# Optimization experiments

Measured on AMD Instinct MI355X. Metric: run time of the kernel, lower is better.

## Reference

```python
import jax, jax.numpy as jnp
import numpy as np

B, S = 64, 1024
ATTEND_DIM = QUERY_DIM = ATT_DIM = 1024


def setup_inputs() -> dict:
    key = jax.random.key(0)
    ks = jax.random.split(key, 8)
    sc_pre = 1.0 / np.sqrt(ATTEND_DIM)
    sc_q = 1.0 / np.sqrt(QUERY_DIM)
    sc_v = 1.0 / np.sqrt(ATT_DIM)
    return {
        "input": jax.random.normal(ks[0], (B, QUERY_DIM), jnp.float32),
        "context": jax.random.normal(ks[1], (B, S, ATTEND_DIM), jnp.float32),
        "coverage_acc": jax.random.uniform(ks[2], (B, S), jnp.float32),
        "W_pre": jax.random.normal(ks[3], (ATT_DIM, ATTEND_DIM), jnp.float32) * sc_pre,
        "b_pre": jax.random.normal(ks[4], (ATT_DIM,), jnp.float32) * sc_pre,
        "W_q": jax.random.normal(ks[5], (ATT_DIM, QUERY_DIM), jnp.float32) * sc_q,
        "W_v": jax.random.normal(ks[6], (1, ATT_DIM), jnp.float32) * sc_v,
        "W_cov": jax.random.normal(ks[7], (ATT_DIM, 1), jnp.float32),
    }


def reference(input, context, coverage_acc, W_pre, b_pre, W_q, W_v, W_cov):
    # precompute = linear_pre(context): (B, S, att_dim)
    precompute = jnp.einsum('bsa,da->bsd', context, W_pre) + b_pre
    # targetT = linear_q(input): (B, 1, att_dim)
    targetT = (input @ W_q.T)[:, None, :]
    # coverage contribution: linear_cov(coverage[..., None]) -> (B, S, att_dim)
    cov_term = coverage_acc[..., None] * W_cov[:, 0]
    tmp = jnp.tanh(precompute + targetT + cov_term)
    # energy = linear_v(tanh(...)): (B, S)
    energy = jnp.einsum('bsd,d->bs', tmp, W_v[0])
    score = jax.nn.softmax(energy, axis=1)
    coverage_new = coverage_acc + score
    weightedContext = jnp.einsum('bs,bsa->ba', score, context)
    return (weightedContext, score, coverage_new, precompute)
```

## Files before the change

kernel.cpp:

```cpp
#include <hip/hip_runtime.h>
#include <hip/hip_bf16.h>

#define B_  64
#define S_  1024
#define D_  1024
#define K_  1024

typedef unsigned short u16;
typedef short bf16x8 __attribute__((ext_vector_type(8)));
typedef float f32x4  __attribute__((ext_vector_type(4)));
typedef u16   u16x8  __attribute__((ext_vector_type(8)));
typedef u16   u16x4  __attribute__((ext_vector_type(4)));

#define WS_TARGET 0
#define WS_EPART  262144
#define WS_WCPART 2359296
#define WS_WPRE   6553600
#define WS_CTXBF  8650752
#define WS_NEED_BF 142868480ull

__device__ __forceinline__ u16 f2bf(float f) {
    unsigned u = __float_as_uint(f);
    return (u16)((u + 0x7fffu + ((u >> 16) & 1u)) >> 16);
}
__device__ __forceinline__ float bf2f(u16 h) {
    return __uint_as_float(((unsigned)h) << 16);
}
__device__ __forceinline__ float fast_tanh(float x) {
    float t = __expf(2.0f * x);
    return 1.0f - 2.0f * __builtin_amdgcn_rcpf(t + 1.0f);
}

__device__ __forceinline__ void glds16(const void* g, void* l) {
    __builtin_amdgcn_global_load_lds(
        (__attribute__((address_space(1))) void*)(size_t)g,
        (__attribute__((address_space(3))) void*)(unsigned int)(size_t)l,
        16, 0, 0);
}

__global__ void convert_bf16x8_kernel(const float* __restrict__ src, u16* __restrict__ dst) {
    size_t i = ((size_t)blockIdx.x * 256 + threadIdx.x) * 8;
    float4 a = *reinterpret_cast<const float4*>(src + i);
    float4 b = *reinterpret_cast<const float4*>(src + i + 4);
    u16x8 h = { f2bf(a.x), f2bf(a.y), f2bf(a.z), f2bf(a.w),
                f2bf(b.x), f2bf(b.y), f2bf(b.z), f2bf(b.w) };
    *reinterpret_cast<u16x8*>(dst + i) = h;
}

__global__ void target_kernel(const float* __restrict__ inp, const float* __restrict__ wq,
                              float* __restrict__ target) {
    int tid  = threadIdx.x;
    int lane = tid & 63, wid = tid >> 6;
    int pair = blockIdx.x * 4 + wid;
    int b = pair & 63, n = pair >> 6;
    const float* ir = inp + (size_t)b * K_;
    const float* wr = wq  + (size_t)n * K_;
    float acc = 0.f;
#pragma unroll
    for (int jj = 0; jj < 4; ++jj) {
        int off = jj * 256 + lane * 4;
        float4 a = *reinterpret_cast<const float4*>(ir + off);
        float4 w = *reinterpret_cast<const float4*>(wr + off);
        acc += a.x * w.x + a.y * w.y + a.z * w.z + a.w * w.w;
    }
#pragma unroll
    for (int off = 1; off < 64; off <<= 1) acc += __shfl_xor(acc, off);
    if (lane == 0) target[pair] = acc;
}

__global__ __launch_bounds__(256, 2)
void gemm_ep_fast(const u16* __restrict__ ctxb, const u16* __restrict__ wpre,
                  const float* __restrict__ bpre, const float* __restrict__ wv,
                  const float* __restrict__ wcov, const float* __restrict__ target,
                  const float* __restrict__ cov, float* __restrict__ pre_out,
                  float* __restrict__ epart) {
    __shared__ __align__(16) u16 As[256 * 32];
    __shared__ __align__(16) u16 Bs[128 * 32];
    __shared__ float esm[256];

    const int tid  = threadIdx.x;
    const int lane = tid & 63;
    const int wid  = tid >> 6;
    const int wm = wid >> 1, wn = wid & 1;
    const int lr = lane & 15, quad = lane >> 4;
    const int m_base = blockIdx.y * 256;
    const int n_base = blockIdx.x * 128;
    const int b      = m_base >> 10;
    const int s_base = m_base & 1023;

    const int srow = lane >> 2;
    const int scol = (lane & 3) * 8;
    const u16* gA = ctxb + (size_t)(m_base + wid * 64 + srow) * K_ + scol;
    const u16* gB = wpre + (size_t)(n_base + wid * 32 + srow) * K_ + scol;
    u16* lA = &As[(wid * 64) * 32];
    u16* lB = &Bs[(wid * 32) * 32];

    f32x4 acc[8][4];
#pragma unroll
    for (int i = 0; i < 8; ++i)
#pragma unroll
        for (int j = 0; j < 4; ++j) acc[i][j] = (f32x4){0.f, 0.f, 0.f, 0.f};

    esm[tid] = 0.0f;

    for (int kt = 0; kt < 32; ++kt) {
        const int k0 = kt * 32;
#pragma unroll
        for (int c = 0; c < 4; ++c)
            glds16(gA + (size_t)(c * 16) * K_ + k0, lA + c * 16 * 32);
#pragma unroll
        for (int c = 0; c < 2; ++c)
            glds16(gB + (size_t)(c * 16) * K_ + k0, lB + c * 16 * 32);
        __syncthreads();

        bf16x8 af[8], bfr[4];
#pragma unroll
        for (int i = 0; i < 8; ++i)
            af[i] = *reinterpret_cast<const bf16x8*>(&As[(wm * 128 + i * 16 + lr) * 32 + quad * 8]);
#pragma unroll
        for (int j = 0; j < 4; ++j)
            bfr[j] = *reinterpret_cast<const bf16x8*>(&Bs[(wn * 64 + j * 16 + lr) * 32 + quad * 8]);
#pragma unroll
        for (int i = 0; i < 8; ++i)
#pragma unroll
            for (int j = 0; j < 4; ++j)
                acc[i][j] = __builtin_amdgcn_mfma_f32_16x16x32_bf16(af[i], bfr[j], acc[i][j], 0, 0, 0);
        __syncthreads();
    }

    float bpre_j[4], wv_j[4], wcov_j[4], tgt_j[4];
    int n_j[4];
#pragma unroll
    for (int j = 0; j < 4; ++j) {
        n_j[j]    = n_base + wn * 64 + j * 16 + lr;
        bpre_j[j] = bpre[n_j[j]];
        wv_j[j]   = wv[n_j[j]];
        wcov_j[j] = wcov[n_j[j]];
        tgt_j[j]  = target[n_j[j] * 64 + b];
    }
#pragma unroll
    for (int i = 0; i < 8; ++i) {
#pragma unroll
        for (int r = 0; r < 4; ++r) {
            int row_local = wm * 128 + i * 16 + quad * 4 + r;
            int m = m_base + row_local;
            int s = s_base + row_local;
            float c = cov[b * S_ + s];
            float esum = 0.f;
#pragma unroll
            for (int j = 0; j < 4; ++j) {
                float pre = acc[i][j][r] + bpre_j[j];
                __builtin_nontemporal_store(pre, &pre_out[(size_t)m * D_ + n_j[j]]);
                float t = fast_tanh(pre + tgt_j[j] + c * wcov_j[j]);
                esum += t * wv_j[j];
            }
            esum += __shfl_xor(esum, 1);
            esum += __shfl_xor(esum, 2);
            esum += __shfl_xor(esum, 4);
            esum += __shfl_xor(esum, 8);
            if (lr == 0) atomicAdd(&esm[row_local], esum);
        }
    }
    __syncthreads();
    epart[(size_t)(m_base + tid) * 8 + blockIdx.x] = esm[tid];
}

#define LDA 40
__global__ __launch_bounds__(256, 2)
void gemm_ep_fallback(const float* __restrict__ ctxf, const u16* __restrict__ wpre,
                      const float* __restrict__ bpre, const float* __restrict__ wv,
                      const float* __restrict__ wcov, const float* __restrict__ target,
                      const float* __restrict__ cov, float* __restrict__ pre_out,
                      float* __restrict__ epart) {
    __shared__ __align__(16) u16 As[256 * LDA];
    __shared__ __align__(16) u16 Bs[128 * LDA];
    __shared__ float esm[256];
    const int tid  = threadIdx.x;
    const int lane = tid & 63;
    const int wid  = tid >> 6;
    const int wm = wid >> 1, wn = wid & 1;
    const int lr = lane & 15, quad = lane >> 4;
    const int m_base = blockIdx.y * 256;
    const int n_base = blockIdx.x * 128;
    const int b      = m_base >> 10;
    const int s_base = m_base & 1023;

    f32x4 acc[8][4];
#pragma unroll
    for (int i = 0; i < 8; ++i)
#pragma unroll
        for (int j = 0; j < 4; ++j) acc[i][j] = (f32x4){0.f, 0.f, 0.f, 0.f};
    esm[tid] = 0.0f;

    for (int kt = 0; kt < 32; ++kt) {
        const int k0 = kt * 32;
        {
            const int row0 = tid >> 3, kc = (tid & 7) * 4;
#pragma unroll
            for (int p = 0; p < 8; ++p) {
                int row = row0 + p * 32;
                float4 v = *reinterpret_cast<const float4*>(
                    ctxf + (size_t)(m_base + row) * K_ + k0 + kc);
                u16x4 h = { f2bf(v.x), f2bf(v.y), f2bf(v.z), f2bf(v.w) };
                *reinterpret_cast<u16x4*>(&As[row * LDA + kc]) = h;
            }
        }
        {
            const int row0 = tid >> 2, kc = (tid & 3) * 8;
#pragma unroll
            for (int p = 0; p < 2; ++p) {
                int row = row0 + p * 64;
                u16x8 v = *reinterpret_cast<const u16x8*>(
                    wpre + (size_t)(n_base + row) * K_ + k0 + kc);
                *reinterpret_cast<u16x8*>(&Bs[row * LDA + kc]) = v;
            }
        }
        __syncthreads();
        bf16x8 af[8], bfr[4];
#pragma unroll
        for (int i = 0; i < 8; ++i)
            af[i] = *reinterpret_cast<const bf16x8*>(&As[(wm * 128 + i * 16 + lr) * LDA + quad * 8]);
#pragma unroll
        for (int j = 0; j < 4; ++j)
            bfr[j] = *reinterpret_cast<const bf16x8*>(&Bs[(wn * 64 + j * 16 + lr) * LDA + quad * 8]);
#pragma unroll
        for (int i = 0; i < 8; ++i)
#pragma unroll
            for (int j = 0; j < 4; ++j)
                acc[i][j] = __builtin_amdgcn_mfma_f32_16x16x32_bf16(af[i], bfr[j], acc[i][j], 0, 0, 0);
        __syncthreads();
    }
    float bpre_j[4], wv_j[4], wcov_j[4], tgt_j[4];
    int n_j[4];
#pragma unroll
    for (int j = 0; j < 4; ++j) {
        n_j[j]    = n_base + wn * 64 + j * 16 + lr;
        bpre_j[j] = bpre[n_j[j]];
        wv_j[j]   = wv[n_j[j]];
        wcov_j[j] = wcov[n_j[j]];
        tgt_j[j]  = target[n_j[j] * 64 + b];
    }
#pragma unroll
    for (int i = 0; i < 8; ++i) {
#pragma unroll
        for (int r = 0; r < 4; ++r) {
            int row_local = wm * 128 + i * 16 + quad * 4 + r;
            int m = m_base + row_local;
            int s = s_base + row_local;
            float c = cov[b * S_ + s];
            float esum = 0.f;
#pragma unroll
            for (int j = 0; j < 4; ++j) {
                float pre = acc[i][j][r] + bpre_j[j];
                __builtin_nontemporal_store(pre, &pre_out[(size_t)m * D_ + n_j[j]]);
                float t = fast_tanh(pre + tgt_j[j] + c * wcov_j[j]);
                esum += t * wv_j[j];
            }
            esum += __shfl_xor(esum, 1);
            esum += __shfl_xor(esum, 2);
            esum += __shfl_xor(esum, 4);
            esum += __shfl_xor(esum, 8);
            if (lr == 0) atomicAdd(&esm[row_local], esum);
        }
    }
    __syncthreads();
    epart[(size_t)(m_base + tid) * 8 + blockIdx.x] = esm[tid];
}

__global__ void softmax_cov_kernel(const float* __restrict__ epart, const float* __restrict__ cov,
                                   float* __restrict__ score, float* __restrict__ covnew) {
    int b = blockIdx.x, t = threadIdx.x;
    int lane = t & 63, wid = t >> 6;
    __shared__ float red[4];
    float e[4];
    float lmax = -3.4e38f;
#pragma unroll
    for (int p = 0; p < 4; ++p) {
        int s = p * 256 + t;
        const float4* q = reinterpret_cast<const float4*>(epart + (size_t)(b * S_ + s) * 8);
        float4 a = q[0], c = q[1];
        e[p] = a.x + a.y + a.z + a.w + c.x + c.y + c.z + c.w;
        lmax = fmaxf(lmax, e[p]);
    }
#pragma unroll
    for (int off = 1; off < 64; off <<= 1) lmax = fmaxf(lmax, __shfl_xor(lmax, off));
    if (lane == 0) red[wid] = lmax;
    __syncthreads();
    float bm = fmaxf(fmaxf(red[0], red[1]), fmaxf(red[2], red[3]));
    __syncthreads();
    float ex[4];
    float lsum = 0.f;
#pragma unroll
    for (int p = 0; p < 4; ++p) { ex[p] = __expf(e[p] - bm); lsum += ex[p]; }
#pragma unroll
    for (int off = 1; off < 64; off <<= 1) lsum += __shfl_xor(lsum, off);
    if (lane == 0) red[wid] = lsum;
    __syncthreads();
    float total = red[0] + red[1] + red[2] + red[3];
    float inv = __builtin_amdgcn_rcpf(total);
#pragma unroll
    for (int p = 0; p < 4; ++p) {
        int s = p * 256 + t;
        float sc = ex[p] * inv;
        score[b * S_ + s]  = sc;
        covnew[b * S_ + s] = cov[b * S_ + s] + sc;
    }
}

__global__ void wc_partial_bf(const float* __restrict__ score, const u16* __restrict__ ctxb,
                              float* __restrict__ part) {
    int sp = blockIdx.x, b = blockIdx.y, t = threadIdx.x;
    int col = t * 4;
    float ax = 0.f, ay = 0.f, az = 0.f, aw = 0.f;
    const u16*   base  = ctxb + ((size_t)b * S_ + sp * 64) * K_ + col;
    const float* sbase = score + b * S_ + sp * 64;
    for (int ss = 0; ss < 64; ++ss) {
        float w = sbase[ss];
        u16x4 c = *reinterpret_cast<const u16x4*>(base + (size_t)ss * K_);
        ax += w * bf2f(c[0]); ay += w * bf2f(c[1]);
        az += w * bf2f(c[2]); aw += w * bf2f(c[3]);
    }
    float4 o = { ax, ay, az, aw };
    *reinterpret_cast<float4*>(part + (size_t)(b * 16 + sp) * 1024 + col) = o;
}

__global__ void wc_partial_f32(const float* __restrict__ score, const float* __restrict__ ctx,
                               float* __restrict__ part) {
    int sp = blockIdx.x, b = blockIdx.y, t = threadIdx.x;
    int col = t * 4;
    float ax = 0.f, ay = 0.f, az = 0.f, aw = 0.f;
    const float* base  = ctx + ((size_t)b * S_ + sp * 64) * K_ + col;
    const float* sbase = score + b * S_ + sp * 64;
    for (int ss = 0; ss < 64; ++ss) {
        float w = sbase[ss];
        float4 c = *reinterpret_cast<const float4*>(base + (size_t)ss * K_);
        ax += w * c.x; ay += w * c.y; az += w * c.z; aw += w * c.w;
    }
    float4 o = { ax, ay, az, aw };
    *reinterpret_cast<float4*>(part + (size_t)(b * 16 + sp) * 1024 + col) = o;
}

__global__ void wc_reduce_kernel(const float* __restrict__ part, float* __restrict__ wc) {
    int b = blockIdx.x, t = threadIdx.x;
    int col = t * 4;
    float ax = 0.f, ay = 0.f, az = 0.f, aw = 0.f;
#pragma unroll
    for (int p = 0; p < 16; ++p) {
        float4 v = *reinterpret_cast<const float4*>(part + (size_t)(b * 16 + p) * 1024 + col);
        ax += v.x; ay += v.y; az += v.z; aw += v.w;
    }
    float4 o = { ax, ay, az, aw };
    *reinterpret_cast<float4*>(wc + b * 1024 + col) = o;
}

extern "C" void kernel_launch(void* const* d_in, const int* in_sizes, int n_in,
                              void* d_out, int out_size, void* d_ws, size_t ws_size,
                              hipStream_t stream) {
    const float* input = (const float*)d_in[0];
    const float* ctx   = (const float*)d_in[1];
    const float* cov   = (const float*)d_in[2];
    const float* Wpre  = (const float*)d_in[3];
    const float* bpre  = (const float*)d_in[4];
    const float* Wq    = (const float*)d_in[5];
    const float* Wv    = (const float*)d_in[6];
    const float* Wcov  = (const float*)d_in[7];

    float* out        = (float*)d_out;
    float* out_wc     = out;
    float* out_score  = out + 65536;
    float* out_covnew = out + 131072;
    float* out_pre    = out + 196608;

    char*  ws        = (char*)d_ws;
    float* ws_target = (float*)(ws + WS_TARGET);
    float* ws_epart  = (float*)(ws + WS_EPART);
    float* ws_wcpart = (float*)(ws + WS_WCPART);
    u16*   ws_wpre   = (u16*)(ws + WS_WPRE);
    u16*   ws_ctxbf  = (u16*)(ws + WS_CTXBF);

    const bool use_bf = (ws_size >= WS_NEED_BF);

    convert_bf16x8_kernel<<<512, 256, 0, stream>>>(Wpre, ws_wpre);
    if (use_bf)
        convert_bf16x8_kernel<<<32768, 256, 0, stream>>>(ctx, ws_ctxbf);
    target_kernel<<<16384, 256, 0, stream>>>(input, Wq, ws_target);
    dim3 ggrid(8, 256);
    if (use_bf)
        gemm_ep_fast<<<ggrid, 256, 0, stream>>>(ws_ctxbf, ws_wpre, bpre, Wv, Wcov,
                                                ws_target, cov, out_pre, ws_epart);
    else
        gemm_ep_fallback<<<ggrid, 256, 0, stream>>>(ctx, ws_wpre, bpre, Wv, Wcov,
                                                    ws_target, cov, out_pre, ws_epart);
    softmax_cov_kernel<<<64, 256, 0, stream>>>(ws_epart, cov, out_score, out_covnew);
    if (use_bf)
        wc_partial_bf<<<dim3(16, 64), 256, 0, stream>>>(out_score, ws_ctxbf, ws_wcpart);
    else
        wc_partial_f32<<<dim3(16, 64), 256, 0, stream>>>(out_score, ctx, ws_wcpart);
    wc_reduce_kernel<<<64, 256, 0, stream>>>(ws_wcpart, out_wc);
}
```

Measured before the change: 694.2 us.

## Double-buffer LDS tiles in fast GEMM and remap blocks for XCD locality

Splits the shared-memory A/B tiles into two buffers so the global-to-LDS load of the next K tile is issued before the MFMA work on the current one. This hides load latency and halves the barriers per K step. It also switches to a 1D grid whose block index is remapped so that the eight N-tiles of one M-tile share an XCD, improving L2 reuse of the context rows. LDS use doubles, which may reduce occupancy under the 2-blocks-per-SM launch bound.

```diff
diff --git a/kernel.cpp b/kernel.cpp
--- a/kernel.cpp
+++ b/kernel.cpp
@@ -74,8 +74,10 @@
                   const float* __restrict__ wcov, const float* __restrict__ target,
                   const float* __restrict__ cov, float* __restrict__ pre_out,
                   float* __restrict__ epart) {
-    __shared__ __align__(16) u16 As[256 * 32];
-    __shared__ __align__(16) u16 Bs[128 * 32];
+    __shared__ __align__(16) u16 As0[256 * 32];
+    __shared__ __align__(16) u16 As1[256 * 32];
+    __shared__ __align__(16) u16 Bs0[128 * 32];
+    __shared__ __align__(16) u16 Bs1[128 * 32];
     __shared__ float esm[256];
 
     const int tid  = threadIdx.x;
@@ -83,8 +85,14 @@
     const int wid  = tid >> 6;
     const int wm = wid >> 1, wn = wid & 1;
     const int lr = lane & 15, quad = lane >> 4;
-    const int m_base = blockIdx.y * 256;
-    const int n_base = blockIdx.x * 128;
+
+    const int lin  = blockIdx.x;
+    const int xcd  = lin & 7;
+    const int slot = lin >> 3;
+    const int mt   = (slot >> 3) * 8 + xcd;
+    const int nt   = slot & 7;
+    const int m_base = mt * 256;
+    const int n_base = nt * 128;
     const int b      = m_base >> 10;
     const int s_base = m_base & 1023;
 
@@ -92,8 +100,10 @@
     const int scol = (lane & 3) * 8;
     const u16* gA = ctxb + (size_t)(m_base + wid * 64 + srow) * K_ + scol;
     const u16* gB = wpre + (size_t)(n_base + wid * 32 + srow) * K_ + scol;
-    u16* lA = &As[(wid * 64) * 32];
-    u16* lB = &Bs[(wid * 32) * 32];
+    u16* lA0 = &As0[(wid * 64) * 32];
+    u16* lA1 = &As1[(wid * 64) * 32];
+    u16* lB0 = &Bs0[(wid * 32) * 32];
+    u16* lB1 = &Bs1[(wid * 32) * 32];
 
     f32x4 acc[8][4];
 #pragma unroll
@@ -103,30 +113,40 @@
 
     esm[tid] = 0.0f;
 
-    for (int kt = 0; kt < 32; ++kt) {
-        const int k0 = kt * 32;
-#pragma unroll
-        for (int c = 0; c < 4; ++c)
-            glds16(gA + (size_t)(c * 16) * K_ + k0, lA + c * 16 * 32);
-#pragma unroll
-        for (int c = 0; c < 2; ++c)
-            glds16(gB + (size_t)(c * 16) * K_ + k0, lB + c * 16 * 32);
+#define STAGE_(k0, lA_, lB_) do {                                              \
+    _Pragma("unroll") for (int c = 0; c < 4; ++c)                              \
+        glds16(gA + (size_t)(c * 16) * K_ + (k0), (lA_) + c * 16 * 32);        \
+    _Pragma("unroll") for (int c = 0; c < 2; ++c)                              \
+        glds16(gB + (size_t)(c * 16) * K_ + (k0), (lB_) + c * 16 * 32);        \
+} while (0)
+
+#define COMPUTE_(AsB, BsB) do {                                                \
+    bf16x8 af[8], bfr[4];                                                      \
+    _Pragma("unroll") for (int i = 0; i < 8; ++i)                              \
+        af[i] = *reinterpret_cast<const bf16x8*>(                              \
+            &(AsB)[(wm * 128 + i * 16 + lr) * 32 + quad * 8]);                 \
+    _Pragma("unroll") for (int j = 0; j < 4; ++j)                              \
+        bfr[j] = *reinterpret_cast<const bf16x8*>(                             \
+            &(BsB)[(wn * 64 + j * 16 + lr) * 32 + quad * 8]);                  \
+    _Pragma("unroll") for (int i = 0; i < 8; ++i)                              \
+        _Pragma("unroll") for (int j = 0; j < 4; ++j)                          \
+            acc[i][j] = __builtin_amdgcn_mfma_f32_16x16x32_bf16(               \
+                af[i], bfr[j], acc[i][j], 0, 0, 0);                            \
+} while (0)
+
+    STAGE_(0, lA0, lB0);
+    __syncthreads();
+
+    for (int kt = 0; kt < 32; kt += 2) {
+        STAGE_((kt + 1) * 32, lA1, lB1);
+        COMPUTE_(As0, Bs0);
         __syncthreads();
-
-        bf16x8 af[8], bfr[4];
-#pragma unroll
-        for (int i = 0; i < 8; ++i)
-            af[i] = *reinterpret_cast<const bf16x8*>(&As[(wm * 128 + i * 16 + lr) * 32 + quad * 8]);
-#pragma unroll
-        for (int j = 0; j < 4; ++j)
-            bfr[j] = *reinterpret_cast<const bf16x8*>(&Bs[(wn * 64 + j * 16 + lr) * 32 + quad * 8]);
-#pragma unroll
-        for (int i = 0; i < 8; ++i)
-#pragma unroll
-            for (int j = 0; j < 4; ++j)
-                acc[i][j] = __builtin_amdgcn_mfma_f32_16x16x32_bf16(af[i], bfr[j], acc[i][j], 0, 0, 0);
+        if (kt < 30) STAGE_((kt + 2) * 32, lA0, lB0);
+        COMPUTE_(As1, Bs1);
         __syncthreads();
     }
+#undef STAGE_
+#undef COMPUTE_
 
     float bpre_j[4], wv_j[4], wcov_j[4], tgt_j[4];
     int n_j[4];
@@ -162,7 +182,7 @@
         }
     }
     __syncthreads();
-    epart[(size_t)(m_base + tid) * 8 + blockIdx.x] = esm[tid];
+    epart[(size_t)(m_base + tid) * 8 + nt] = esm[tid];
 }
 
 #define LDA 40
@@ -384,13 +404,14 @@
     if (use_bf)
         convert_bf16x8_kernel<<<32768, 256, 0, stream>>>(ctx, ws_ctxbf);
     target_kernel<<<16384, 256, 0, stream>>>(input, Wq, ws_target);
-    dim3 ggrid(8, 256);
     if (use_bf)
-        gemm_ep_fast<<<ggrid, 256, 0, stream>>>(ws_ctxbf, ws_wpre, bpre, Wv, Wcov,
-                                                ws_target, cov, out_pre, ws_epart);
-    else
+        gemm_ep_fast<<<2048, 256, 0, stream>>>(ws_ctxbf, ws_wpre, bpre, Wv, Wcov,
+                                               ws_target, cov, out_pre, ws_epart);
+    else {
+        dim3 ggrid(8, 256);
         gemm_ep_fallback<<<ggrid, 256, 0, stream>>>(ctx, ws_wpre, bpre, Wv, Wcov,
                                                     ws_target, cov, out_pre, ws_epart);
+    }
     softmax_cov_kernel<<<64, 256, 0, stream>>>(ws_epart, cov, out_score, out_covnew);
     if (use_bf)
         wc_partial_bf<<<dim3(16, 64), 256, 0, stream>>>(out_score, ws_ctxbf, ws_wcpart);
```

After: 659.6 us. -5.0%, faster.

## Shrink GEMM tile to 128x128, swizzle LDS, remap blocks across XCDs

Applied to the files above, without the earlier changes.

The fused GEMM+energy kernel drops from 256x128 to 128x128 output tiles and raises the occupancy hint to three blocks per SM. It adds an XOR swizzle on the LDS column index to cut bank conflicts on MFMA fragment loads. It also uses a 1D grid with an XCD-aware mapping so blocks sharing A rows run on the same XCD and reuse L2. Smaller tiles mean more loads of the B operand per FLOP but lower register pressure and better latency hiding.

```diff
diff --git a/kernel.cpp b/kernel.cpp
--- a/kernel.cpp
+++ b/kernel.cpp
@@ -68,63 +68,71 @@
     if (lane == 0) target[pair] = acc;
 }
 
-__global__ __launch_bounds__(256, 2)
+__global__ __launch_bounds__(256, 3)
 void gemm_ep_fast(const u16* __restrict__ ctxb, const u16* __restrict__ wpre,
                   const float* __restrict__ bpre, const float* __restrict__ wv,
                   const float* __restrict__ wcov, const float* __restrict__ target,
                   const float* __restrict__ cov, float* __restrict__ pre_out,
                   float* __restrict__ epart) {
-    __shared__ __align__(16) u16 As[256 * 32];
+    __shared__ __align__(16) u16 As[128 * 32];
     __shared__ __align__(16) u16 Bs[128 * 32];
-    __shared__ float esm[256];
+    __shared__ float esm[128];
 
     const int tid  = threadIdx.x;
     const int lane = tid & 63;
     const int wid  = tid >> 6;
     const int wm = wid >> 1, wn = wid & 1;
     const int lr = lane & 15, quad = lane >> 4;
-    const int m_base = blockIdx.y * 256;
-    const int n_base = blockIdx.x * 128;
+    const int sq = quad ^ ((lr >> 1) & 3);
+
+    const int lin  = blockIdx.x;
+    const int xcd  = lin & 7;
+    const int slot = lin >> 3;
+    const int mt   = (slot >> 3) * 8 + xcd;
+    const int nt   = slot & 7;
+    const int m_base = mt * 128;
+    const int n_base = nt * 128;
     const int b      = m_base >> 10;
     const int s_base = m_base & 1023;
 
     const int srow = lane >> 2;
-    const int scol = (lane & 3) * 8;
-    const u16* gA = ctxb + (size_t)(m_base + wid * 64 + srow) * K_ + scol;
+    const int scol = ((lane & 3) ^ ((lane >> 3) & 3)) * 8;
+    const u16* gA = ctxb + (size_t)(m_base + wid * 32 + srow) * K_ + scol;
     const u16* gB = wpre + (size_t)(n_base + wid * 32 + srow) * K_ + scol;
-    u16* lA = &As[(wid * 64) * 32];
+    u16* lA = &As[(wid * 32) * 32];
     u16* lB = &Bs[(wid * 32) * 32];
 
-    f32x4 acc[8][4];
-#pragma unroll
-    for (int i = 0; i < 8; ++i)
+    f32x4 acc[4][4];
+#pragma unroll
+    for (int i = 0; i < 4; ++i)
 #pragma unroll
         for (int j = 0; j < 4; ++j) acc[i][j] = (f32x4){0.f, 0.f, 0.f, 0.f};
 
-    esm[tid] = 0.0f;
+    if (tid < 128) esm[tid] = 0.0f;
 
     for (int kt = 0; kt < 32; ++kt) {
         const int k0 = kt * 32;
-#pragma unroll
-        for (int c = 0; c < 4; ++c)
-            glds16(gA + (size_t)(c * 16) * K_ + k0, lA + c * 16 * 32);
-#pragma unroll
-        for (int c = 0; c < 2; ++c)
-            glds16(gB + (size_t)(c * 16) * K_ + k0, lB + c * 16 * 32);
+        glds16(gA + k0,                      lA);
+        glds16(gA + (size_t)16 * K_ + k0,    lA + 16 * 32);
+        glds16(gB + k0,                      lB);
+        glds16(gB + (size_t)16 * K_ + k0,    lB + 16 * 32);
         __syncthreads();
 
-        bf16x8 af[8], bfr[4];
-#pragma unroll
-        for (int i = 0; i < 8; ++i)
-            af[i] = *reinterpret_cast<const bf16x8*>(&As[(wm * 128 + i * 16 + lr) * 32 + quad * 8]);
+        bf16x8 af[4], bfr[4];
+#pragma unroll
+        for (int i = 0; i < 4; ++i)
+            af[i] = *reinterpret_cast<const bf16x8*>(
+                &As[(wm * 64 + i * 16 + lr) * 32 + sq * 8]);
 #pragma unroll
         for (int j = 0; j < 4; ++j)
-            bfr[j] = *reinterpret_cast<const bf16x8*>(&Bs[(wn * 64 + j * 16 + lr) * 32 + quad * 8]);
-#pragma unroll
-        for (int i = 0; i < 8; ++i)
+            bfr[j] = *reinterpret_cast<const bf16x8*>(
+                &Bs[(wn * 64 + j * 16 + lr) * 32 + sq * 8]);
+#pragma unroll
+        for (int i = 0; i < 4; ++i)
 #pragma unroll
             for (int j = 0; j < 4; ++j)
-                acc[i][j] = __builtin_amdgcn_mfma_f32_16x16x32_bf16(af[i], bfr[j], acc[i][j], 0, 0, 0);
+                acc[i][j] = __builtin_amdgcn_mfma_f32_16x16x32_bf16(
+                    af[i], bfr[j], acc[i][j], 0, 0, 0);
         __syncthreads();
     }
 
@@ -139,10 +147,10 @@
         tgt_j[j]  = target[n_j[j] * 64 + b];
     }
 #pragma unroll
-    for (int i = 0; i < 8; ++i) {
+    for (int i = 0; i < 4; ++i) {
 #pragma unroll
         for (int r = 0; r < 4; ++r) {
-            int row_local = wm * 128 + i * 16 + quad * 4 + r;
+            int row_local = wm * 64 + i * 16 + quad * 4 + r;
             int m = m_base + row_local;
             int s = s_base + row_local;
             float c = cov[b * S_ + s];
@@ -162,7 +170,7 @@
         }
     }
     __syncthreads();
-    epart[(size_t)(m_base + tid) * 8 + blockIdx.x] = esm[tid];
+    if (tid < 128) epart[(size_t)(m_base + tid) * 8 + nt] = esm[tid];
 }
 
 #define LDA 40
@@ -384,13 +392,14 @@
     if (use_bf)
         convert_bf16x8_kernel<<<32768, 256, 0, stream>>>(ctx, ws_ctxbf);
     target_kernel<<<16384, 256, 0, stream>>>(input, Wq, ws_target);
-    dim3 ggrid(8, 256);
     if (use_bf)
-        gemm_ep_fast<<<ggrid, 256, 0, stream>>>(ws_ctxbf, ws_wpre, bpre, Wv, Wcov,
-                                                ws_target, cov, out_pre, ws_epart);
-    else
+        gemm_ep_fast<<<4096, 256, 0, stream>>>(ws_ctxbf, ws_wpre, bpre, Wv, Wcov,
+                                               ws_target, cov, out_pre, ws_epart);
+    else {
+        dim3 ggrid(8, 256);
         gemm_ep_fallback<<<ggrid, 256, 0, stream>>>(ctx, ws_wpre, bpre, Wv, Wcov,
                                                     ws_target, cov, out_pre, ws_epart);
+    }
     softmax_cov_kernel<<<64, 256, 0, stream>>>(ws_epart, cov, out_score, out_covnew);
     if (use_bf)
         wc_partial_bf<<<dim3(16, 64), 256, 0, stream>>>(out_score, ws_ctxbf, ws_wcpart);
```

New measurement: 669.4 us. 3.6% less time.

## Restructure fused GEMM into 256x256 double-buffered ping-pong pipeline with XCD-aware tiling

Applied to the files above, without the earlier changes.

The fused precompute GEMM+energy kernel moves to 512-thread blocks computing 256x256 tiles with K-step 64. The tiles are double-buffered in LDS with XOR-swizzled layout, and global-to-LDS loads are interleaved with MFMA phases using explicit barriers, waitcnt and setprio. Block IDs are remapped so consecutive M tiles are spread across XCDs for better L2 reuse of the B operand. This aims to hide load latency and cut LDS bank conflicts and global traffic. In exchange it brings heavy LDS use (128KB), fragile manual synchronization, and epart padding with zeros for unused slots.

```diff
diff --git a/kernel.cpp b/kernel.cpp
--- a/kernel.cpp
+++ b/kernel.cpp
@@ -68,32 +68,38 @@
     if (lane == 0) target[pair] = acc;
 }
 
-__global__ __launch_bounds__(256, 2)
+__global__ __launch_bounds__(512, 2)
 void gemm_ep_fast(const u16* __restrict__ ctxb, const u16* __restrict__ wpre,
                   const float* __restrict__ bpre, const float* __restrict__ wv,
                   const float* __restrict__ wcov, const float* __restrict__ target,
                   const float* __restrict__ cov, float* __restrict__ pre_out,
                   float* __restrict__ epart) {
-    __shared__ __align__(16) u16 As[256 * 32];
-    __shared__ __align__(16) u16 Bs[128 * 32];
+    __shared__ __align__(16) u16 A0[256 * 64];
+    __shared__ __align__(16) u16 A1[256 * 64];
+    __shared__ __align__(16) u16 B0[256 * 64];
+    __shared__ __align__(16) u16 B1[256 * 64];
     __shared__ float esm[256];
 
     const int tid  = threadIdx.x;
     const int lane = tid & 63;
     const int wid  = tid >> 6;
-    const int wm = wid >> 1, wn = wid & 1;
+    const int wm = wid >> 2, wn = wid & 3;
     const int lr = lane & 15, quad = lane >> 4;
-    const int m_base = blockIdx.y * 256;
-    const int n_base = blockIdx.x * 128;
+
+    const int lin  = blockIdx.x;
+    const int xcd  = lin & 7;
+    const int slot = lin >> 3;
+    const int nt   = slot & 3;
+    const int mt   = (slot >> 2) * 8 + xcd;
+    const int m_base = mt * 256;
+    const int n_base = nt * 256;
     const int b      = m_base >> 10;
     const int s_base = m_base & 1023;
 
-    const int srow = lane >> 2;
-    const int scol = (lane & 3) * 8;
-    const u16* gA = ctxb + (size_t)(m_base + wid * 64 + srow) * K_ + scol;
-    const u16* gB = wpre + (size_t)(n_base + wid * 32 + srow) * K_ + scol;
-    u16* lA = &As[(wid * 64) * 32];
-    u16* lB = &Bs[(wid * 32) * 32];
+    const int srow8 = lane >> 3;
+    const int scol  = ((lane & 7) ^ (lane >> 3)) * 8;
+    const u16* gA = ctxb + (size_t)(m_base + wid * 16 + srow8) * K_ + scol;
+    const u16* gB = wpre + (size_t)(n_base + wid * 16 + srow8) * K_ + scol;
 
     f32x4 acc[8][4];
 #pragma unroll
@@ -101,32 +107,94 @@
 #pragma unroll
         for (int j = 0; j < 4; ++j) acc[i][j] = (f32x4){0.f, 0.f, 0.f, 0.f};
 
-    esm[tid] = 0.0f;
-
-    for (int kt = 0; kt < 32; ++kt) {
-        const int k0 = kt * 32;
-#pragma unroll
-        for (int c = 0; c < 4; ++c)
-            glds16(gA + (size_t)(c * 16) * K_ + k0, lA + c * 16 * 32);
-#pragma unroll
-        for (int c = 0; c < 2; ++c)
-            glds16(gB + (size_t)(c * 16) * K_ + k0, lB + c * 16 * 32);
-        __syncthreads();
-
-        bf16x8 af[8], bfr[4];
-#pragma unroll
-        for (int i = 0; i < 8; ++i)
-            af[i] = *reinterpret_cast<const bf16x8*>(&As[(wm * 128 + i * 16 + lr) * 32 + quad * 8]);
-#pragma unroll
-        for (int j = 0; j < 4; ++j)
-            bfr[j] = *reinterpret_cast<const bf16x8*>(&Bs[(wn * 64 + j * 16 + lr) * 32 + quad * 8]);
-#pragma unroll
-        for (int i = 0; i < 8; ++i)
-#pragma unroll
-            for (int j = 0; j < 4; ++j)
-                acc[i][j] = __builtin_amdgcn_mfma_f32_16x16x32_bf16(af[i], bfr[j], acc[i][j], 0, 0, 0);
-        __syncthreads();
-    }
+#define STG(garr, R, kt_, larr) do {                                           \
+    glds16(garr + (size_t)(R) * K_ + (kt_) * 64,                               \
+           &larr[((R) + wid * 16 + 0) * 64]);                                  \
+    glds16(garr + (size_t)((R) + 8) * K_ + (kt_) * 64,                         \
+           &larr[((R) + wid * 16 + 8) * 64]);                                  \
+} while (0)
+
+#define LDA4(dst, arr, ibase, h)                                               \
+    _Pragma("unroll") for (int ii = 0; ii < 4; ++ii)                           \
+        dst[ii] = *reinterpret_cast<const bf16x8*>(                            \
+            &arr[(wm * 128 + ((ibase) + ii) * 16 + lr) * 64 +                  \
+                 ((((h) * 4 + quad) ^ (lr & 7)) * 8)]);
+#define LDB4(dst, arr, h)                                                      \
+    _Pragma("unroll") for (int jj = 0; jj < 4; ++jj)                           \
+        dst[jj] = *reinterpret_cast<const bf16x8*>(                            \
+            &arr[(wn * 64 + jj * 16 + lr) * 64 +                               \
+                 ((((h) * 4 + quad) ^ (lr & 7)) * 8)]);
+#define MFMA16(ibase, A4, B4)                                                  \
+    _Pragma("unroll") for (int ii = 0; ii < 4; ++ii)                           \
+        _Pragma("unroll") for (int jj = 0; jj < 4; ++jj)                       \
+            acc[(ibase) + ii][jj] = __builtin_amdgcn_mfma_f32_16x16x32_bf16(   \
+                A4[ii], B4[jj], acc[(ibase) + ii][jj], 0, 0, 0);
+
+#define PH_MID() do {                                                          \
+    __builtin_amdgcn_s_barrier();                                              \
+    asm volatile("s_waitcnt lgkmcnt(0)" ::: "memory");                         \
+    __builtin_amdgcn_sched_barrier(0);                                         \
+    __builtin_amdgcn_s_setprio(1);                                             \
+} while (0)
+#define PH_END() do {                                                          \
+    __builtin_amdgcn_s_setprio(0);                                             \
+    __builtin_amdgcn_s_barrier();                                              \
+    __builtin_amdgcn_sched_barrier(0);                                         \
+} while (0)
+#define PH_END_VM() do {                                                       \
+    __builtin_amdgcn_s_setprio(0);                                             \
+    asm volatile("s_waitcnt vmcnt(2)" ::: "memory");                           \
+    __builtin_amdgcn_s_barrier();                                              \
+    __builtin_amdgcn_sched_barrier(0);                                         \
+} while (0)
+
+    bf16x8 alo[4], ahi[4], bfv[4];
+
+    STG(gA, 0, 0, A0); STG(gA, 128, 0, A0);
+    STG(gB, 0, 0, B0); STG(gB, 128, 0, B0);
+    STG(gB, 0, 1, B1);
+    if (tid < 256) esm[tid] = 0.0f;
+    asm volatile("s_waitcnt vmcnt(2)" ::: "memory");
+    __builtin_amdgcn_s_barrier();
+    __builtin_amdgcn_sched_barrier(0);
+
+    for (int i = 0; i < 8; ++i) {
+        const int t1 = 2 * i + 1;
+        const int t2 = (2 * i + 2 < 16) ? 2 * i + 2 : 15;
+        const int t3 = (2 * i + 3 < 16) ? 2 * i + 3 : 15;
+        LDA4(alo, A0, 0, 0); LDB4(bfv, B0, 0);
+        STG(gA, 0, t1, A1);
+        PH_MID(); MFMA16(0, alo, bfv); PH_END();
+        LDA4(ahi, A0, 4, 0);
+        STG(gA, 128, t1, A1);
+        PH_MID(); MFMA16(4, ahi, bfv); PH_END();
+        LDA4(alo, A0, 0, 1); LDB4(bfv, B0, 1);
+        STG(gB, 128, t1, B1);
+        PH_MID(); MFMA16(0, alo, bfv); PH_END();
+        LDA4(ahi, A0, 4, 1);
+        STG(gB, 0, t2, B0);
+        PH_MID(); MFMA16(4, ahi, bfv); PH_END_VM();
+        LDA4(alo, A1, 0, 0); LDB4(bfv, B1, 0);
+        STG(gA, 0, t2, A0);
+        PH_MID(); MFMA16(0, alo, bfv); PH_END();
+        LDA4(ahi, A1, 4, 0);
+        STG(gA, 128, t2, A0);
+        PH_MID(); MFMA16(4, ahi, bfv); PH_END();
+        LDA4(alo, A1, 0, 1); LDB4(bfv, B1, 1);
+        STG(gB, 128, t2, B0);
+        PH_MID(); MFMA16(0, alo, bfv); PH_END();
+        LDA4(ahi, A1, 4, 1);
+        STG(gB, 0, t3, B1);
+        PH_MID(); MFMA16(4, ahi, bfv); PH_END_VM();
+    }
+    asm volatile("s_waitcnt vmcnt(0)" ::: "memory");
+#undef STG
+#undef LDA4
+#undef LDB4
+#undef MFMA16
+#undef PH_MID
+#undef PH_END
+#undef PH_END_VM
 
     float bpre_j[4], wv_j[4], wcov_j[4], tgt_j[4];
     int n_j[4];
@@ -162,7 +230,10 @@
         }
     }
     __syncthreads();
-    epart[(size_t)(m_base + tid) * 8 + blockIdx.x] = esm[tid];
+    if (tid < 256) {
+        epart[(size_t)(m_base + tid) * 8 + nt]     = esm[tid];
+        epart[(size_t)(m_base + tid) * 8 + nt + 4] = 0.0f;
+    }
 }
 
 #define LDA 40
@@ -384,13 +455,14 @@
     if (use_bf)
         convert_bf16x8_kernel<<<32768, 256, 0, stream>>>(ctx, ws_ctxbf);
     target_kernel<<<16384, 256, 0, stream>>>(input, Wq, ws_target);
-    dim3 ggrid(8, 256);
     if (use_bf)
-        gemm_ep_fast<<<ggrid, 256, 0, stream>>>(ws_ctxbf, ws_wpre, bpre, Wv, Wcov,
-                                                ws_target, cov, out_pre, ws_epart);
-    else
+        gemm_ep_fast<<<1024, 512, 0, stream>>>(ws_ctxbf, ws_wpre, bpre, Wv, Wcov,
+                                               ws_target, cov, out_pre, ws_epart);
+    else {
+        dim3 ggrid(8, 256);
         gemm_ep_fallback<<<ggrid, 256, 0, stream>>>(ctx, ws_wpre, bpre, Wv, Wcov,
                                                     ws_target, cov, out_pre, ws_epart);
+    }
     softmax_cov_kernel<<<64, 256, 0, stream>>>(ws_epart, cov, out_score, out_covnew);
     if (use_bf)
         wc_partial_bf<<<dim3(16, 64), 256, 0, stream>>>(out_score, ws_ctxbf, ws_wcpart);
```

New measurement: 641.1 us. 7.6% less time.
